# Performance work log

Measured on AMD Instinct MI355X. Metric: run time of the kernel, lower is better.

The kernel has to match this reference:

```python
import jax, jax.numpy as jnp
import numpy as np

B, S, D, H, DK, DV = 4, 1024, 1024, 16, 64, 64
HALF = D // 2            # 512
DKH = DK // 2            # per-head half q/k dim = 32
DVH = DV // 2            # per-head half v dim = 32


def setup_inputs() -> dict:
    key = jax.random.key(0)
    ks = jax.random.split(key, 12)
    f = lambda k, sh: jax.random.normal(k, sh, dtype=jnp.float32)
    inp = {
        "input_Q": f(ks[0], (B, S, D)),
        "input_K": f(ks[1], (B, S, D)),
        "input_V": f(ks[2], (B, S, D)),
    }
    # causal mask (True = masked), matching attn_mask() helper for non-pad tokens
    causal = jnp.triu(jnp.ones((S, S), dtype=bool), k=1)
    inp["attn_mask"] = jnp.broadcast_to(causal, (B, S, S))
    scale = 0.02
    # projections: [in=HALF, out=DK*H//2=HALF] stored as (in, out) for x @ W
    for i, n in enumerate(["WQ1", "WK1", "WV1", "WQ2", "WK2", "WV2"]):
        inp[n] = f(ks[3 + i], (HALF, DK * H // 2)) * scale
    inp["Wfc1"] = f(ks[9], (H * DV // 2, HALF)) * scale
    inp["Wfc2"] = f(ks[10], (H * DV // 2, HALF)) * scale
    inp["ln_g"] = jnp.ones((HALF,), dtype=jnp.float32)
    inp["ln_b"] = jnp.zeros((HALF,), dtype=jnp.float32)
    return inp


def _layernorm(x, g, b, eps=1e-5):
    mu = jnp.mean(x, axis=-1, keepdims=True)
    var = jnp.mean((x - mu) ** 2, axis=-1, keepdims=True)
    return (x - mu) * jax.lax.rsqrt(var + eps) * g + b


def _heads(x, dh):
    # [B, S, H*dh] -> [B, H, S, dh]
    return x.reshape(B, S, H, dh).transpose(0, 2, 1, 3)


def reference(input_Q, input_K, input_V, attn_mask,
              WQ1, WK1, WV1, WQ2, WK2, WV2, Wfc1, Wfc2, ln_g, ln_b):
    res1 = input_Q[:, :, :HALF]
    res2 = input_Q[:, :, HALF:]
    # half-dim projections, split into heads
    Q1 = _heads(input_Q[:, :, :HALF] @ WQ1, DKH)   # [B,H,S,DKH]
    K1 = _heads(input_K[:, :, :HALF] @ WK1, DKH)
    V1 = _heads(input_V[:, :, :HALF] @ WV1, DVH)
    V2 = _heads(input_V[:, :, HALF:] @ WV2, DVH)
    # Q2/K2 are computed in the original but unused by the attention scores;
    # still compute them for faithfulness (they'd carry grads of zero).
    _Q2 = _heads(input_Q[:, :, HALF:] @ WQ2, DKH)
    _K2 = _heads(input_K[:, :, HALF:] @ WK2, DKH)
    V = jnp.concatenate([V1, V2], axis=-1)         # [B,H,S,DV]
    # attention scores from half-dim Q1/K1 only, scaled by sqrt(d_k//2)
    attn = jnp.einsum("bhqd,bhkd->bhqk", Q1, K1) / np.sqrt(DKH).astype(np.float32)
    masked = jnp.where(attn_mask[:, None, :, :], jnp.float32(-1e9), attn)
    softmax_attn = jax.nn.softmax(masked, axis=-1)  # [B,H,S,S]
    qkv = jnp.einsum("bhqk,bhkd->bhqd", softmax_attn, V)  # [B,H,S,DV]
    qkv_out = qkv.transpose(0, 2, 1, 3).reshape(B, S, H * DV)
    out1 = _layernorm(qkv_out[:, :, : H * DV // 2] @ Wfc1 + res1, ln_g, ln_b)
    out2 = _layernorm(qkv_out[:, :, H * DV // 2 :] @ Wfc2 + res2, ln_g, ln_b)
    output = jnp.concatenate([out1, out2], axis=-1)
    return output, softmax_attn
```

## Files before the change

kernel.cpp:

```cpp
#include <hip/hip_runtime.h>

typedef unsigned short u16;
typedef __attribute__((ext_vector_type(8))) short bf16x8;
typedef __attribute__((ext_vector_type(4))) float f32x4;
typedef __attribute__((ext_vector_type(4))) unsigned short u16x4;

#define B_    4
#define S_    1024
#define D_    1024
#define H_    16
#define BS_   4096
#define HALF_ 512


__device__ __forceinline__ u16 f2b(float f){
    unsigned u; __builtin_memcpy(&u, &f, 4);
    u += 0x7fffu + ((u >> 16) & 1u);
    return (u16)(u >> 16);
}

__global__ __launch_bounds__(256) void k_transpose(
    const float* w0, const float* w1, const float* w2, const float* w3,
    const float* w4, const float* w5, u16* out)
{
    __shared__ u16 tile[32][33];
    const float* src;
    switch (blockIdx.z) {
        case 0: src = w0; break; case 1: src = w1; break; case 2: src = w2; break;
        case 3: src = w3; break; case 4: src = w4; break; default: src = w5; break;
    }
    u16* dst = out + (size_t)blockIdx.z * 512 * 512;
    int tx = threadIdx.x & 31, ty = threadIdx.x >> 5;
    int x = blockIdx.x * 32 + tx;
    #pragma unroll
    for (int j = 0; j < 32; j += 8)
        tile[ty + j][tx] = f2b(src[(size_t)(blockIdx.y * 32 + ty + j) * 512 + x]);
    __syncthreads();
    int x2 = blockIdx.y * 32 + tx;
    #pragma unroll
    for (int j = 0; j < 32; j += 8)
        dst[(size_t)(blockIdx.x * 32 + ty + j) * 512 + x2] = tile[tx][ty + j];
}

__global__ __launch_bounds__(256) void k_proj(
    const float* Q, const float* K, const float* V, const u16* WT,
    u16* Qh, u16* Kh, u16* Vt)
{
    __shared__ u16 tile[64][72];
    int which = blockIdx.z;
    const float* X; const u16* Wt; int xofs;
    if      (which == 0) { X = Q; Wt = WT + 0*512*512; xofs = 0;   }
    else if (which == 1) { X = K; Wt = WT + 1*512*512; xofs = 0;   }
    else if (which == 2) { X = V; Wt = WT + 2*512*512; xofs = 0;   }
    else                 { X = V; Wt = WT + 3*512*512; xofs = 512; }

    int lane = threadIdx.x & 63, w = threadIdx.x >> 6;
    int l15 = lane & 15, quad = lane >> 4;
    int m0 = blockIdx.x * 64 + w * 16;
    int n0 = blockIdx.y * 64;

    f32x4 acc[4] = {{0,0,0,0},{0,0,0,0},{0,0,0,0},{0,0,0,0}};
    const float* arow = X + (size_t)(m0 + l15) * D_ + xofs + quad * 8;

    for (int k0 = 0; k0 < 512; k0 += 32) {
        float4 fa = *(const float4*)(arow + k0);
        float4 fb = *(const float4*)(arow + k0 + 4);
        bf16x8 a;
        a[0] = (short)f2b(fa.x); a[1] = (short)f2b(fa.y);
        a[2] = (short)f2b(fa.z); a[3] = (short)f2b(fa.w);
        a[4] = (short)f2b(fb.x); a[5] = (short)f2b(fb.y);
        a[6] = (short)f2b(fb.z); a[7] = (short)f2b(fb.w);
        #pragma unroll
        for (int nt = 0; nt < 4; nt++) {
            bf16x8 b = *(const bf16x8*)(Wt + (size_t)(n0 + nt*16 + l15) * 512 + k0 + quad * 8);
            acc[nt] = __builtin_amdgcn_mfma_f32_16x16x32_bf16(a, b, acc[nt], 0, 0, 0);
        }
    }

    if (which <= 1) {
        #pragma unroll
        for (int nt = 0; nt < 4; nt++) {
            #pragma unroll
            for (int r = 0; r < 4; r++) {
                int m = m0 + quad * 4 + r;
                int n = n0 + nt * 16 + l15;
                int b = m >> 10, s = m & 1023;
                int h = n >> 5,  d = n & 31;
                u16 v = f2b(acc[nt][r]);
                if (which == 0) Qh[(((size_t)(b*16 + h))*1024 + s)*32 + d] = v;
                else            Kh[(((size_t)(b*16 + h))*1024 + s)*32 + d] = v;
            }
        }
    } else {
        #pragma unroll
        for (int nt = 0; nt < 4; nt++)
            #pragma unroll
            for (int r = 0; r < 4; r++)
                tile[nt*16 + l15][w*16 + quad*4 + r] = f2b(acc[nt][r]);
        __syncthreads();
        int nl = threadIdx.x >> 2;
        int s4 = (threadIdx.x & 3) * 16;
        int n  = n0 + nl;
        int h  = n >> 5;
        int dv = (n & 31) + (which == 3 ? 32 : 0);
        int M0 = blockIdx.x * 64;
        int b  = M0 >> 10;
        u16* dst = Vt + (((size_t)(b*16 + h)) * 64 + dv) * 1024 + (M0 & 1023) + s4;
        *(bf16x8*)dst       = *(const bf16x8*)&tile[nl][s4];
        *(bf16x8*)(dst + 8) = *(const bf16x8*)&tile[nl][s4 + 8];
    }
}

__global__ __launch_bounds__(256) void k_attn(
    const u16* Qh, const u16* Kh, const u16* Vt, float* Pout, u16* QKV)
{
    int bh = blockIdx.y;
    int m0 = blockIdx.x * 16;
    int lane = threadIdx.x & 63, w = threadIdx.x >> 6;
    int l15 = lane & 15, quad = lane >> 4;
    __shared__ float red_max[4][16], red_sum[4][16];
    __shared__ __align__(16) char smem[32768];
    u16   (*pb)[16][256] = (u16 (*)[16][256])smem;
    float (*qred)[16][64] = (float (*)[16][64])smem;

    bf16x8 aq = *(const bf16x8*)(Qh + ((size_t)bh * 1024 + m0 + l15) * 32 + quad * 8);

    float sc[16][4];
    #pragma unroll
    for (int t = 0; t < 16; t++) {
        int n0 = w * 256 + t * 16;
        if (n0 > m0 + 15) {
            #pragma unroll
            for (int r = 0; r < 4; r++) sc[t][r] = -1e30f;
            continue;
        }
        bf16x8 b = *(const bf16x8*)(Kh + ((size_t)bh * 1024 + n0 + l15) * 32 + quad * 8);
        f32x4 z = {0,0,0,0};
        f32x4 c = __builtin_amdgcn_mfma_f32_16x16x32_bf16(aq, b, z, 0, 0, 0);
        int col = n0 + l15;
        #pragma unroll
        for (int r = 0; r < 4; r++) {
            int row = m0 + quad * 4 + r;
            sc[t][r] = (col > row) ? -1e30f : c[r] * 0.17677669529663687f;
        }
    }

    float lmax[4];
    #pragma unroll
    for (int r = 0; r < 4; r++) {
        float m = -1e30f;
        #pragma unroll
        for (int t = 0; t < 16; t++) m = fmaxf(m, sc[t][r]);
        lmax[r] = m;
    }
    #pragma unroll
    for (int mk = 1; mk < 16; mk <<= 1)
        #pragma unroll
        for (int r = 0; r < 4; r++) lmax[r] = fmaxf(lmax[r], __shfl_xor(lmax[r], mk));

    float lsum[4] = {0, 0, 0, 0};
    #pragma unroll
    for (int t = 0; t < 16; t++)
        #pragma unroll
        for (int r = 0; r < 4; r++) {
            float e = __expf(sc[t][r] - lmax[r]);
            sc[t][r] = e; lsum[r] += e;
        }
    #pragma unroll
    for (int mk = 1; mk < 16; mk <<= 1)
        #pragma unroll
        for (int r = 0; r < 4; r++) lsum[r] += __shfl_xor(lsum[r], mk);

    if (l15 == 0)
        #pragma unroll
        for (int r = 0; r < 4; r++) {
            red_max[w][quad * 4 + r] = lmax[r];
            red_sum[w][quad * 4 + r] = lsum[r];
        }
    __syncthreads();

    #pragma unroll
    for (int r = 0; r < 4; r++) {
        int row = quad * 4 + r;
        float ma = red_max[0][row], mb = red_max[1][row];
        float mc = red_max[2][row], md = red_max[3][row];
        float g  = fmaxf(fmaxf(ma, mb), fmaxf(mc, md));
        float tot = __expf(ma - g) * red_sum[0][row] + __expf(mb - g) * red_sum[1][row]
                  + __expf(mc - g) * red_sum[2][row] + __expf(md - g) * red_sum[3][row];
        float fac = __expf(lmax[r] - g) / tot;
        size_t rowbase = ((size_t)bh * 1024 + m0 + row) * 1024 + w * 256 + l15;
        #pragma unroll
        for (int t = 0; t < 16; t++) {
            float val = sc[t][r] * fac;
            Pout[rowbase + t * 16] = val;
            pb[w][row][(t * 16 + l15) ^ ((row & 7) << 3)] = f2b(val);
        }
    }

    f32x4 acc[4] = {{0,0,0,0},{0,0,0,0},{0,0,0,0},{0,0,0,0}};
    int kmax = m0 + 15;
    #pragma unroll
    for (int ks = 0; ks < 8; ks++) {
        int k0 = w * 256 + ks * 32;
        if (k0 <= kmax) {
            bf16x8 a = *(const bf16x8*)(&pb[w][l15][(ks * 32 + quad * 8) ^ ((l15 & 7) << 3)]);
            #pragma unroll
            for (int nt = 0; nt < 4; nt++) {
                bf16x8 bv = *(const bf16x8*)(Vt + ((size_t)bh * 64 + nt * 16 + l15) * 1024 + k0 + quad * 8);
                acc[nt] = __builtin_amdgcn_mfma_f32_16x16x32_bf16(a, bv, acc[nt], 0, 0, 0);
            }
        }
    }

    __syncthreads();
    #pragma unroll
    for (int nt = 0; nt < 4; nt++)
        #pragma unroll
        for (int r = 0; r < 4; r++)
            qred[w][quad * 4 + r][nt * 16 + l15] = acc[nt][r];
    __syncthreads();

    int row = threadIdx.x >> 4;
    int dv4 = (threadIdx.x & 15) * 4;
    float4 q0 = *(const float4*)&qred[0][row][dv4];
    float4 q1 = *(const float4*)&qred[1][row][dv4];
    float4 q2 = *(const float4*)&qred[2][row][dv4];
    float4 q3 = *(const float4*)&qred[3][row][dv4];
    int b = bh >> 4, h = bh & 15;
    u16x4 o;
    o.x = f2b(q0.x + q1.x + q2.x + q3.x);
    o.y = f2b(q0.y + q1.y + q2.y + q3.y);
    o.z = f2b(q0.z + q1.z + q2.z + q3.z);
    o.w = f2b(q0.w + q1.w + q2.w + q3.w);
    *(u16x4*)(QKV + ((size_t)b * 1024 + m0 + row) * 1024 + h * 64 + dv4) = o;
}

__global__ __launch_bounds__(256) void k_fc(
    const u16* QKV, const u16* WT, const float* resQ,
    const float* lng, const float* lnb, float* out)
{
    int half = blockIdx.y;
    int m0 = blockIdx.x * 16;
    int lane = threadIdx.x & 63, w = threadIdx.x >> 6;
    int l15 = lane & 15, quad = lane >> 4;
    __shared__ float red_s[4][16], red_q[4][16];

    const u16* Wt = WT + (size_t)(4 + half) * 512 * 512;
    f32x4 acc[8] = {{0,0,0,0},{0,0,0,0},{0,0,0,0},{0,0,0,0},
                    {0,0,0,0},{0,0,0,0},{0,0,0,0},{0,0,0,0}};
    const u16* arow = QKV + (size_t)(m0 + l15) * 1024 + half * 512 + quad * 8;

    for (int k0 = 0; k0 < 512; k0 += 32) {
        bf16x8 a = *(const bf16x8*)(arow + k0);
        #pragma unroll
        for (int f = 0; f < 8; f++) {
            int n = w * 128 + f * 16 + l15;
            bf16x8 b = *(const bf16x8*)(Wt + (size_t)n * 512 + k0 + quad * 8);
            acc[f] = __builtin_amdgcn_mfma_f32_16x16x32_bf16(a, b, acc[f], 0, 0, 0);
        }
    }

    #pragma unroll
    for (int f = 0; f < 8; f++)
        #pragma unroll
        for (int r = 0; r < 4; r++) {
            int row = m0 + quad * 4 + r;
            int col = w * 128 + f * 16 + l15;
            acc[f][r] += resQ[(size_t)row * 1024 + half * 512 + col];
        }

    float psum[4] = {0,0,0,0}, psq[4] = {0,0,0,0};
    #pragma unroll
    for (int f = 0; f < 8; f++)
        #pragma unroll
        for (int r = 0; r < 4; r++) { psum[r] += acc[f][r]; psq[r] += acc[f][r] * acc[f][r]; }
    #pragma unroll
    for (int mk = 1; mk < 16; mk <<= 1)
        #pragma unroll
        for (int r = 0; r < 4; r++) {
            psum[r] += __shfl_xor(psum[r], mk);
            psq[r]  += __shfl_xor(psq[r],  mk);
        }
    if (l15 == 0)
        #pragma unroll
        for (int r = 0; r < 4; r++) { red_s[w][quad*4+r] = psum[r]; red_q[w][quad*4+r] = psq[r]; }
    __syncthreads();

    #pragma unroll
    for (int r = 0; r < 4; r++) {
        int row = quad * 4 + r;
        float s  = red_s[0][row] + red_s[1][row] + red_s[2][row] + red_s[3][row];
        float q  = red_q[0][row] + red_q[1][row] + red_q[2][row] + red_q[3][row];
        float mu = s * (1.f / 512.f);
        float var = fmaxf(q * (1.f / 512.f) - mu * mu, 0.f);
        float rstd = rsqrtf(var + 1e-5f);
        #pragma unroll
        for (int f = 0; f < 8; f++) {
            int col = w * 128 + f * 16 + l15;
            float g = lng[col], bb = lnb[col];
            float v = (acc[f][r] - mu) * rstd * g + bb;
            out[(size_t)(m0 + row) * 1024 + half * 512 + col] = v;
        }
    }
}

extern "C" void kernel_launch(void* const* d_in, const int* in_sizes, int n_in,
                              void* d_out, int out_size, void* d_ws, size_t ws_size,
                              hipStream_t stream)
{
    const float* Q    = (const float*)d_in[0];
    const float* K    = (const float*)d_in[1];
    const float* V    = (const float*)d_in[2];
    const float* WQ1  = (const float*)d_in[4];
    const float* WK1  = (const float*)d_in[5];
    const float* WV1  = (const float*)d_in[6];
    const float* WV2  = (const float*)d_in[9];
    const float* Wfc1 = (const float*)d_in[10];
    const float* Wfc2 = (const float*)d_in[11];
    const float* lng  = (const float*)d_in[12];
    const float* lnb  = (const float*)d_in[13];

    float* out   = (float*)d_out;
    u16*   ws16  = (u16*)d_ws;
    u16*   WT    = ws16;
    u16*   QKV   = ws16 + 1572864;

    u16*   Vt    = (u16*)out;
    u16*   Qh    = (u16*)(out + 2097152);
    u16*   Kh    = (u16*)(out + 3145728);
    float* attn  = out + (size_t)BS_ * D_;

    k_transpose<<<dim3(16, 16, 6), 256, 0, stream>>>(WQ1, WK1, WV1, WV2, Wfc1, Wfc2, WT);
    k_proj     <<<dim3(64, 8, 4),  256, 0, stream>>>(Q, K, V, WT, Qh, Kh, Vt);
    k_attn     <<<dim3(64, 64),    256, 0, stream>>>(Qh, Kh, Vt, attn, QKV);
    k_fc       <<<dim3(256, 2),    256, 0, stream>>>(QKV, WT, Q, lng, lnb, out);
}
```

Before: 546.4 us.

## Transpose QK^T MFMA so each lane owns a query row, vectorize P stores

Swaps the MFMA operand order so the score tile comes out transposed, giving each lane four consecutive key columns of a single query row. The row max and sum then take only two cross-lane shuffles instead of a 4-step butterfly per row. The softmax output is written as 16-byte nontemporal float4 stores, and the bf16 copy goes to LDS as 8-byte stores, replacing scalar writes. This is meant to cut the shuffle work and the number of store instructions, at the cost of changing the LDS write pattern under the existing swizzle.

```diff
diff --git a/kernel.cpp b/kernel.cpp
--- a/kernel.cpp
+++ b/kernel.cpp
@@ -123,7 +123,8 @@
     u16   (*pb)[16][256] = (u16 (*)[16][256])smem;
     float (*qred)[16][64] = (float (*)[16][64])smem;
 
-    bf16x8 aq = *(const bf16x8*)(Qh + ((size_t)bh * 1024 + m0 + l15) * 32 + quad * 8);
+    bf16x8 bq = *(const bf16x8*)(Qh + ((size_t)bh * 1024 + m0 + l15) * 32 + quad * 8);
+    int qrow = m0 + l15;
 
     float sc[16][4];
     #pragma unroll
@@ -134,67 +135,56 @@
             for (int r = 0; r < 4; r++) sc[t][r] = -1e30f;
             continue;
         }
-        bf16x8 b = *(const bf16x8*)(Kh + ((size_t)bh * 1024 + n0 + l15) * 32 + quad * 8);
+        bf16x8 ak = *(const bf16x8*)(Kh + ((size_t)bh * 1024 + n0 + l15) * 32 + quad * 8);
         f32x4 z = {0,0,0,0};
-        f32x4 c = __builtin_amdgcn_mfma_f32_16x16x32_bf16(aq, b, z, 0, 0, 0);
-        int col = n0 + l15;
+        f32x4 c = __builtin_amdgcn_mfma_f32_16x16x32_bf16(ak, bq, z, 0, 0, 0);
         #pragma unroll
         for (int r = 0; r < 4; r++) {
-            int row = m0 + quad * 4 + r;
-            sc[t][r] = (col > row) ? -1e30f : c[r] * 0.17677669529663687f;
-        }
-    }
-
-    float lmax[4];
-    #pragma unroll
-    for (int r = 0; r < 4; r++) {
-        float m = -1e30f;
-        #pragma unroll
-        for (int t = 0; t < 16; t++) m = fmaxf(m, sc[t][r]);
-        lmax[r] = m;
-    }
-    #pragma unroll
-    for (int mk = 1; mk < 16; mk <<= 1)
-        #pragma unroll
-        for (int r = 0; r < 4; r++) lmax[r] = fmaxf(lmax[r], __shfl_xor(lmax[r], mk));
-
-    float lsum[4] = {0, 0, 0, 0};
+            int col = n0 + quad * 4 + r;
+            sc[t][r] = (col > qrow) ? -1e30f : c[r] * 0.17677669529663687f;
+        }
+    }
+
+    float m = -1e30f;
     #pragma unroll
     for (int t = 0; t < 16; t++)
         #pragma unroll
+        for (int r = 0; r < 4; r++) m = fmaxf(m, sc[t][r]);
+    m = fmaxf(m, __shfl_xor(m, 16));
+    m = fmaxf(m, __shfl_xor(m, 32));
+
+    float s = 0.f;
+    #pragma unroll
+    for (int t = 0; t < 16; t++)
+        #pragma unroll
         for (int r = 0; r < 4; r++) {
-            float e = __expf(sc[t][r] - lmax[r]);
-            sc[t][r] = e; lsum[r] += e;
-        }
-    #pragma unroll
-    for (int mk = 1; mk < 16; mk <<= 1)
-        #pragma unroll
-        for (int r = 0; r < 4; r++) lsum[r] += __shfl_xor(lsum[r], mk);
-
-    if (l15 == 0)
-        #pragma unroll
-        for (int r = 0; r < 4; r++) {
-            red_max[w][quad * 4 + r] = lmax[r];
-            red_sum[w][quad * 4 + r] = lsum[r];
-        }
-    __syncthreads();
-
-    #pragma unroll
-    for (int r = 0; r < 4; r++) {
-        int row = quad * 4 + r;
-        float ma = red_max[0][row], mb = red_max[1][row];
-        float mc = red_max[2][row], md = red_max[3][row];
-        float g  = fmaxf(fmaxf(ma, mb), fmaxf(mc, md));
-        float tot = __expf(ma - g) * red_sum[0][row] + __expf(mb - g) * red_sum[1][row]
-                  + __expf(mc - g) * red_sum[2][row] + __expf(md - g) * red_sum[3][row];
-        float fac = __expf(lmax[r] - g) / tot;
-        size_t rowbase = ((size_t)bh * 1024 + m0 + row) * 1024 + w * 256 + l15;
-        #pragma unroll
-        for (int t = 0; t < 16; t++) {
-            float val = sc[t][r] * fac;
-            Pout[rowbase + t * 16] = val;
-            pb[w][row][(t * 16 + l15) ^ ((row & 7) << 3)] = f2b(val);
-        }
+            float e = __expf(sc[t][r] - m);
+            sc[t][r] = e; s += e;
+        }
+    s += __shfl_xor(s, 16);
+    s += __shfl_xor(s, 32);
+
+    if (lane < 16) { red_max[w][l15] = m; red_sum[w][l15] = s; }
+    __syncthreads();
+
+    float ma = red_max[0][l15], mb = red_max[1][l15];
+    float mc = red_max[2][l15], md = red_max[3][l15];
+    float g  = fmaxf(fmaxf(ma, mb), fmaxf(mc, md));
+    float tot = __expf(ma - g) * red_sum[0][l15] + __expf(mb - g) * red_sum[1][l15]
+              + __expf(mc - g) * red_sum[2][l15] + __expf(md - g) * red_sum[3][l15];
+    float fac = __expf(m - g) / tot;
+
+    size_t rowbase = ((size_t)bh * 1024 + qrow) * 1024 + w * 256 + quad * 4;
+    int swz = (l15 & 7) << 3;
+    #pragma unroll
+    for (int t = 0; t < 16; t++) {
+        f32x4 v;
+        v[0] = sc[t][0] * fac; v[1] = sc[t][1] * fac;
+        v[2] = sc[t][2] * fac; v[3] = sc[t][3] * fac;
+        __builtin_nontemporal_store(v, (f32x4*)(Pout + rowbase + t * 16));
+        u16x4 pv;
+        pv.x = f2b(v[0]); pv.y = f2b(v[1]); pv.z = f2b(v[2]); pv.w = f2b(v[3]);
+        *(u16x4*)&pb[w][l15][(t * 16 + quad * 4) ^ swz] = pv;
     }
 
     f32x4 acc[4] = {{0,0,0,0},{0,0,0,0},{0,0,0,0},{0,0,0,0}};
```

Measured after the change: 533.2 us. 2.4% less time.
